# Kernel optimization log

Measured on AMD Instinct MI355X. Metric: run time of the kernel, lower is better.

## Reference

```python
import jax, jax.numpy as jnp
import numpy as np
from jax import lax

NUM_TAGS = 9
HIDDEN = 768
BATCH = 64
SEQ = 512


def setup_inputs() -> dict:
    key = jax.random.key(0)
    ks = jax.random.split(key, 6)
    hidden = jax.random.normal(ks[0], (BATCH, SEQ, HIDDEN), dtype=jnp.float32)
    labels = jax.random.randint(ks[1], (BATCH, SEQ), 0, NUM_TAGS)  # all >= 0 -> full mask
    weight = jax.random.normal(ks[2], (NUM_TAGS, HIDDEN), dtype=jnp.float32) * 0.02
    bias = jnp.zeros((NUM_TAGS,), dtype=jnp.float32)
    start_transitions = jax.random.normal(ks[3], (NUM_TAGS,), dtype=jnp.float32) * 0.1
    end_transitions = jax.random.normal(ks[4], (NUM_TAGS,), dtype=jnp.float32) * 0.1
    transitions = jax.random.normal(ks[5], (NUM_TAGS, NUM_TAGS), dtype=jnp.float32) * 0.1
    return dict(hidden=hidden, labels=labels, weight=weight, bias=bias,
                start_transitions=start_transitions, end_transitions=end_transitions,
                transitions=transitions)


def _crf_log_likelihood(emissions, tags, mask, start_t, end_t, trans):
    """pytorch-crf log-likelihood, reduction='sum'.
    emissions [B,L,T] float, tags [B,L] int, mask [B,L] bool."""
    # --- numerator: score of the gold path ---
    tag0 = tags[:, 0]
    score0 = start_t[tag0] + jnp.take_along_axis(emissions[:, 0], tag0[:, None], axis=1)[:, 0]

    def num_step(carry, inp):
        score, prev = carry
        em, tg, m = inp  # em [B,T], tg [B], m [B]
        s = trans[prev, tg] + jnp.take_along_axis(em, tg[:, None], axis=1)[:, 0]
        score = score + jnp.where(m, s, jnp.zeros_like(s))
        prev = jnp.where(m, tg, prev)
        return (score, prev), None

    (num_score, last_tag), _ = lax.scan(
        num_step, (score0, tag0),
        (emissions[:, 1:].swapaxes(0, 1), tags[:, 1:].T, mask[:, 1:].T))
    numerator = num_score + end_t[last_tag]

    # --- denominator: forward algorithm (log-sum-exp recurrence) ---
    alpha0 = start_t[None, :] + emissions[:, 0]  # [B,T]

    def den_step(alpha, inp):
        em, m = inp  # em [B,T], m [B]
        nxt = jax.nn.logsumexp(alpha[:, :, None] + trans[None], axis=1) + em
        alpha = jnp.where(m[:, None], nxt, alpha)
        return alpha, None

    alpha, _ = lax.scan(den_step, alpha0,
                        (emissions[:, 1:].swapaxes(0, 1), mask[:, 1:].T))
    denominator = jax.nn.logsumexp(alpha + end_t[None, :], axis=1)

    return jnp.sum(numerator - denominator)


def _viterbi_decode(emissions, mask, start_t, end_t, trans):
    """Max-plus DP + backtrack. Returns padded [B,L] int32 best tag sequence."""
    B, L, T = emissions.shape
    score0 = start_t[None, :] + emissions[:, 0]  # [B,T]
    identity = jnp.arange(T, dtype=jnp.int32)[None, :]  # identity backpointer for masked steps

    def fwd_step(score, inp):
        em, m = inp  # em [B,T], m [B]
        br = score[:, :, None] + trans[None]  # [B,T_prev,T_cur]
        idx = jnp.argmax(br, axis=1).astype(jnp.int32)  # [B,T]
        nxt = jnp.max(br, axis=1) + em
        score = jnp.where(m[:, None], nxt, score)
        idx = jnp.where(m[:, None], idx, identity)
        return score, idx

    final, hist = lax.scan(fwd_step, score0,
                           (emissions[:, 1:].swapaxes(0, 1), mask[:, 1:].T))
    last_tag = jnp.argmax(final + end_t[None, :], axis=1).astype(jnp.int32)  # [B]

    def back_step(tag, idx):  # idx [B,T] backpointers for this position
        prev = jnp.take_along_axis(idx, tag[:, None], axis=1)[:, 0]
        return prev, tag

    first_tag, tags_rev = lax.scan(back_step, last_tag, hist, reverse=True)
    tags = jnp.concatenate([first_tag[None, :], tags_rev], axis=0).T  # [B,L]
    return tags * mask.astype(jnp.int32)


def reference(hidden, labels, weight, bias, start_transitions, end_transitions, transitions):
    mask_full = labels >= 0
    h = hidden[:, 1:-1, :]                       # drop [CLS]/[SEP] positions
    tags = labels[:, 1:-1] * mask_full[:, 1:-1]  # zero out padded labels
    mask = mask_full[:, 1:-1]
    # dropout is identity in eval mode
    emissions = jnp.einsum('blh,th->blt', h, weight) + bias  # [B,L,T]
    llh = _crf_log_likelihood(emissions, tags, mask,
                              start_transitions, end_transitions, transitions)
    tag_seqs = _viterbi_decode(emissions, mask,
                               start_transitions, end_transitions, transitions)
    return -llh, tag_seqs.astype(jnp.float32)
```

## Files before the change

### kernel.cpp

```cpp
#include <hip/hip_runtime.h>
#include <stdint.h>

#define NB 64
#define SEQL 512
#define L 510
#define T 9
#define H 768
#define EMS 12
#define WST 388
#define LN2 0.6931471805599453f

__device__ __forceinline__ float rl(float v, int l) {
  return __uint_as_float(__builtin_amdgcn_readlane(__float_as_uint(v), l));
}

__global__ __launch_bounds__(256) void emis_kernel(
    const float* __restrict__ hidden, const float* __restrict__ weight,
    const float* __restrict__ bias, float* __restrict__ em,
    float* __restrict__ out) {
  __shared__ float4 wl[1728];
  const float4* w4 = (const float4*)weight;
  for (int k = threadIdx.x; k < 1728; k += 256) wl[k] = w4[k];
  if (blockIdx.x == 0 && threadIdx.x == 0) out[0] = 0.f;
  __syncthreads();
  const int lane = threadIdx.x & 63;
  const int wv = threadIdx.x >> 6;
  const int base = blockIdx.x * 32 + wv * 8;
  const float bj = bias[lane < 9 ? lane : 0];

  float4 ha[3], hb[3];
  {
    const int r0 = base, r1 = base + 1;
    const int b0 = r0 / L, p0 = r0 - b0 * L;
    const int b1 = r1 / L, p1 = r1 - b1 * L;
    const float4* h0 = (const float4*)(hidden + ((size_t)(b0 * SEQL + p0 + 1)) * H);
    const float4* h1 = (const float4*)(hidden + ((size_t)(b1 * SEQL + p1 + 1)) * H);
#pragma unroll
    for (int k = 0; k < 3; ++k) { ha[k] = h0[lane + 64 * k]; hb[k] = h1[lane + 64 * k]; }
  }
#pragma unroll 1
  for (int pr = 0; pr < 4; ++pr) {
    const int r0 = base + pr * 2, r1 = r0 + 1;
    float4 na[3], nb[3];
    if (pr < 3) {
      const int q0 = r0 + 2, q1 = r0 + 3;
      const int c0 = q0 / L, s0 = q0 - c0 * L;
      const int c1 = q1 / L, s1 = q1 - c1 * L;
      const float4* h0 = (const float4*)(hidden + ((size_t)(c0 * SEQL + s0 + 1)) * H);
      const float4* h1 = (const float4*)(hidden + ((size_t)(c1 * SEQL + s1 + 1)) * H);
#pragma unroll
      for (int k = 0; k < 3; ++k) { na[k] = h0[lane + 64 * k]; nb[k] = h1[lane + 64 * k]; }
    }
    float a0[T], a1[T];
#pragma unroll
    for (int t = 0; t < T; ++t) { a0[t] = 0.f; a1[t] = 0.f; }
#pragma unroll
    for (int t = 0; t < T; ++t) {
#pragma unroll
      for (int k = 0; k < 3; ++k) {
        float4 w = wl[t * 192 + lane + 64 * k];
        a0[t] = fmaf(ha[k].x, w.x, fmaf(ha[k].y, w.y, fmaf(ha[k].z, w.z, fmaf(ha[k].w, w.w, a0[t]))));
        a1[t] = fmaf(hb[k].x, w.x, fmaf(hb[k].y, w.y, fmaf(hb[k].z, w.z, fmaf(hb[k].w, w.w, a1[t]))));
      }
    }
#pragma unroll
    for (int off = 32; off; off >>= 1) {
#pragma unroll
      for (int t = 0; t < T; ++t) {
        a0[t] += __shfl_xor(a0[t], off);
        a1[t] += __shfl_xor(a1[t], off);
      }
    }
    float v0 = a0[0], v1 = a1[0];
#pragma unroll
    for (int t = 1; t < T; ++t) {
      v0 = (lane == t) ? a0[t] : v0;
      v1 = (lane == t) ? a1[t] : v1;
    }
    if (lane < 9) {
      em[(size_t)r0 * EMS + lane] = v0 + bj;
      em[(size_t)r1 * EMS + lane] = v1 + bj;
    }
#pragma unroll
    for (int k = 0; k < 3; ++k) { ha[k] = na[k]; hb[k] = nb[k]; }
  }
}

__global__ __launch_bounds__(256) void kb_kernel(
    const float* __restrict__ em, const int* __restrict__ labels,
    const float* __restrict__ start_t, const float* __restrict__ end_t,
    const float* __restrict__ trans, float* __restrict__ out) {
  __shared__ float s_emb[16 * WST];
  __shared__ float s_pd[1296];
  __shared__ float s_mv[1296];
  __shared__ float s_A[153];
  __shared__ float s_t[81];
  __shared__ float s_np[4];
  __shared__ int s_lab[L];
  __shared__ unsigned char s_ch[32];
  __shared__ uint32_t s_bp[32 * 16 * 2];
  const int b = blockIdx.x;
  const int tid = threadIdx.x;

  for (int k = tid; k < 81; k += 256) s_t[k] = trans[k];
  for (int k = tid; k < L; k += 256) s_lab[k] = labels[b * SEQL + 1 + k];
  for (int idx = tid; idx < 16 * 32 * 3; idx += 256) {
    const int s = idx / 96, rem = idx - 96 * s;
    const int r = rem / 3, c = rem - 3 * r;
    const int row = 32 * s + 1 + r;
    if (row < L) {
      float4 v = *(const float4*)(em + ((size_t)(b * L + row)) * EMS + c * 4);
      *(float4*)(s_emb + s * WST + r * 12 + c * 4) = v;
    }
  }
  __syncthreads();

  float part = 0.f;
  for (int l = tid; l < L; l += 256) {
    int tg = s_lab[l];
    float e = em[((size_t)(b * L + l)) * EMS + tg];
    if (l == 0) part += start_t[tg] + e;
    else part += s_t[s_lab[l - 1] * 9 + tg] + e;
    if (l == L - 1) part += end_t[tg];
  }
#pragma unroll
  for (int off = 32; off; off >>= 1) part += __shfl_xor(part, off);
  if ((tid & 63) == 0) s_np[tid >> 6] = part;

  const int lane = tid & 63, wv = tid >> 6;
  const int g = lane / 9;
  const int i9 = lane - g * 9;
  const bool act = g < 4;
  const int sw = wv * 4 + (act ? g : 0);
  const int ntw = (sw == 15) ? 29 : 32;
  const float* ew = s_emb + sw * WST;

  {
    float E[81];
#pragma unroll
    for (int k = 0; k < 81; ++k) E[k] = __expf(trans[k]);
    float R[9];
#pragma unroll
    for (int j = 0; j < 9; ++j) R[j] = E[i9 * 9 + j] * __expf(ew[j]);
    int iexp = 0;
    for (int t = 1; t < ntw; ++t) {
      float e[9];
#pragma unroll
      for (int j = 0; j < 9; ++j) e[j] = __expf(ew[t * 12 + j]);
      float Rn[9];
#pragma unroll
      for (int j = 0; j < 9; ++j) {
        float a = R[0] * E[0 * 9 + j];
#pragma unroll
        for (int k = 1; k < 9; ++k) a = fmaf(R[k], E[k * 9 + j], a);
        Rn[j] = a;
      }
#pragma unroll
      for (int j = 0; j < 9; ++j) R[j] = Rn[j] * e[j];
      if ((t & 3) == 0) {
        float mx = R[0];
#pragma unroll
        for (int j = 1; j < 9; ++j) mx = fmaxf(mx, R[j]);
        int ex = (int)((__float_as_uint(mx) >> 23) & 0xff) - 127;
        iexp += ex;
        float sc = __uint_as_float((uint32_t)(127 - ex) << 23);
#pragma unroll
        for (int j = 0; j < 9; ++j) R[j] *= sc;
      }
    }
    if (act) {
      float ls = (float)iexp * LN2;
#pragma unroll
      for (int j = 0; j < 9; ++j)
        s_pd[sw * 81 + j * 9 + i9] = __logf(R[j]) + ls;
    }
  }
  {
    float V[9];
#pragma unroll
    for (int j = 0; j < 9; ++j) V[j] = trans[i9 * 9 + j] + ew[j];
    for (int t = 1; t < ntw; ++t) {
      float Vn[9];
#pragma unroll
      for (int j = 0; j < 9; ++j) {
        float m = V[0] + trans[0 * 9 + j];
#pragma unroll
        for (int k = 1; k < 9; ++k) m = fmaxf(m, V[k] + trans[k * 9 + j]);
        Vn[j] = m + ew[t * 12 + j];
      }
#pragma unroll
      for (int j = 0; j < 9; ++j) V[j] = Vn[j];
    }
    if (act) {
#pragma unroll
      for (int j = 0; j < 9; ++j) s_mv[sw * 81 + j * 9 + i9] = V[j];
    }
  }
  __syncthreads();

  if (tid < 64) {
    const int jj = lane < 9 ? lane : 8;
    float D = start_t[jj] + em[(size_t)b * L * EMS + jj];
    for (int s = 0; s < 16; ++s) {
      const float* col = &s_pd[s * 81 + jj * 9];
      float v0 = rl(D, 0) + col[0], v1 = rl(D, 1) + col[1], v2 = rl(D, 2) + col[2];
      float v3 = rl(D, 3) + col[3], v4 = rl(D, 4) + col[4], v5 = rl(D, 5) + col[5];
      float v6 = rl(D, 6) + col[6], v7 = rl(D, 7) + col[7], v8 = rl(D, 8) + col[8];
      float mx = fmaxf(fmaxf(fmaxf(fmaxf(v0, v1), fmaxf(v2, v3)),
                             fmaxf(fmaxf(v4, v5), fmaxf(v6, v7))), v8);
      float sum = __expf(v0 - mx) + __expf(v1 - mx) + __expf(v2 - mx) +
                  __expf(v3 - mx) + __expf(v4 - mx) + __expf(v5 - mx) +
                  __expf(v6 - mx) + __expf(v7 - mx) + __expf(v8 - mx);
      D = mx + __logf(sum);
    }
    float fe = D + end_t[jj];
    float w0 = rl(fe, 0), w1 = rl(fe, 1), w2 = rl(fe, 2), w3 = rl(fe, 3);
    float w4 = rl(fe, 4), w5 = rl(fe, 5), w6 = rl(fe, 6), w7 = rl(fe, 7), w8 = rl(fe, 8);
    float mx = fmaxf(fmaxf(fmaxf(fmaxf(w0, w1), fmaxf(w2, w3)),
                           fmaxf(fmaxf(w4, w5), fmaxf(w6, w7))), w8);
    float den = mx + __logf(__expf(w0 - mx) + __expf(w1 - mx) + __expf(w2 - mx) +
                            __expf(w3 - mx) + __expf(w4 - mx) + __expf(w5 - mx) +
                            __expf(w6 - mx) + __expf(w7 - mx) + __expf(w8 - mx));
    if (lane == 0)
      atomicAdd(out, den - (s_np[0] + s_np[1] + s_np[2] + s_np[3]));

    float A = start_t[jj] + em[(size_t)b * L * EMS + jj];
    if (lane < 9) s_A[lane] = A;
    for (int s = 0; s < 16; ++s) {
      const float* col = &s_mv[s * 81 + jj * 9];
      float u0 = rl(A, 0) + col[0], u1 = rl(A, 1) + col[1], u2 = rl(A, 2) + col[2];
      float u3 = rl(A, 3) + col[3], u4 = rl(A, 4) + col[4], u5 = rl(A, 5) + col[5];
      float u6 = rl(A, 6) + col[6], u7 = rl(A, 7) + col[7], u8 = rl(A, 8) + col[8];
      A = fmaxf(fmaxf(fmaxf(fmaxf(u0, u1), fmaxf(u2, u3)),
                      fmaxf(fmaxf(u4, u5), fmaxf(u6, u7))), u8);
      if (lane < 9) s_A[(s + 1) * 9 + lane] = A;
    }
    float fv = A + end_t[jj];
    int j = 0;
    {
      float bv = rl(fv, 0);
#pragma unroll
      for (int i = 1; i < 9; ++i) { float v = rl(fv, i); if (v > bv) { bv = v; j = i; } }
    }
    for (int s = 15; s >= 0; --s) {
      float val = s_A[s * 9 + jj] + s_mv[s * 81 + j * 9 + jj];
      int ii = 0;
      float bb = rl(val, 0);
#pragma unroll
      for (int i = 1; i < 9; ++i) { float v = rl(val, i); if (v > bb) { bb = v; ii = i; } }
      if (lane == 0) {
        s_ch[s * 2] = (unsigned char)ii;
        s_ch[s * 2 + 1] = (unsigned char)j;
      }
      j = ii;
    }
    if (lane == 0) out[1 + (size_t)b * L] = (float)j;
  }
  __syncthreads();

  if (tid < 16) {
    const int s = tid;
    const int nt = (s == 15) ? 29 : 32;
    const int l0 = 32 * s + 1;
    const int i0 = s_ch[s * 2];
    const int jF = s_ch[s * 2 + 1];
    const float* ep = s_emb + s * WST;
    float a[9];
#pragma unroll
    for (int jx = 0; jx < 9; ++jx) a[jx] = trans[i0 * 9 + jx] + ep[jx];
    for (int q = 1; q < nt; ++q) {
      uint32_t pk0 = 0, pk1 = 0;
      float an[9];
#pragma unroll
      for (int jx = 0; jx < 9; ++jx) {
        float best = a[0] + trans[0 * 9 + jx];
        int bi = 0;
#pragma unroll
        for (int k = 1; k < 9; ++k) {
          float v = a[k] + trans[k * 9 + jx];
          if (v > best) { best = v; bi = k; }
        }
        an[jx] = best + ep[q * 12 + jx];
        if (jx < 8) pk0 |= ((uint32_t)bi) << (4 * jx);
        else pk1 = (uint32_t)bi;
      }
      s_bp[(q * 16 + s) * 2] = pk0;
      s_bp[(q * 16 + s) * 2 + 1] = pk1;
#pragma unroll
      for (int jx = 0; jx < 9; ++jx) a[jx] = an[jx];
    }
    int cur = jF;
    float* orow = out + 1 + (size_t)b * L + l0;
    for (int q = nt - 1; q >= 1; --q) {
      orow[q] = (float)cur;
      uint32_t pk = s_bp[(q * 16 + s) * 2 + (cur >> 3)];
      cur = (int)((pk >> ((cur & 7) * 4)) & 15u);
    }
    orow[0] = (float)cur;
  }
}

extern "C" void kernel_launch(void* const* d_in, const int* in_sizes, int n_in,
                              void* d_out, int out_size, void* d_ws, size_t ws_size,
                              hipStream_t stream) {
  const float* hidden  = (const float*)d_in[0];
  const int*   labels  = (const int*)d_in[1];
  const float* weight  = (const float*)d_in[2];
  const float* bias    = (const float*)d_in[3];
  const float* start_t = (const float*)d_in[4];
  const float* end_t   = (const float*)d_in[5];
  const float* trans   = (const float*)d_in[6];
  float* out = (float*)d_out;

  float* em = (float*)d_ws;

  emis_kernel<<<1020, 256, 0, stream>>>(hidden, weight, bias, em, out);
  kb_kernel<<<NB, 256, 0, stream>>>(em, labels, start_t, end_t, trans, out);
}
```

Baseline: 233.6 us.

## Run CRF sum-product and max-product chunk scans on separate waves in parallel

The kb kernel now runs 512 threads per block. The first four waves compute the log-space forward chunk matrices and the other four compute the Viterbi max-plus chunk matrices at the same time, where before one set of waves did both one after the other. Both chunk recurrences now start from an identity matrix, and the Viterbi waves cache the transition matrix in registers. The gold-path score now reads emissions from shared memory instead of global memory. The cost is a larger block and register pressure from the 81-entry arrays, and the unchanged later code in the hidden section still has to match the new wave count.

```diff
diff --git a/kernel.cpp b/kernel.cpp
--- a/kernel.cpp
+++ b/kernel.cpp
@@ -86,7 +86,7 @@
   }
 }
 
-__global__ __launch_bounds__(256) void kb_kernel(
+__global__ __launch_bounds__(512, 2) void kb_kernel(
     const float* __restrict__ em, const int* __restrict__ labels,
     const float* __restrict__ start_t, const float* __restrict__ end_t,
     const float* __restrict__ trans, float* __restrict__ out) {
@@ -95,16 +95,16 @@
   __shared__ float s_mv[1296];
   __shared__ float s_A[153];
   __shared__ float s_t[81];
-  __shared__ float s_np[4];
+  __shared__ float s_np[8];
   __shared__ int s_lab[L];
   __shared__ unsigned char s_ch[32];
   __shared__ uint32_t s_bp[32 * 16 * 2];
   const int b = blockIdx.x;
   const int tid = threadIdx.x;
 
-  for (int k = tid; k < 81; k += 256) s_t[k] = trans[k];
-  for (int k = tid; k < L; k += 256) s_lab[k] = labels[b * SEQL + 1 + k];
-  for (int idx = tid; idx < 16 * 32 * 3; idx += 256) {
+  for (int k = tid; k < 81; k += 512) s_t[k] = trans[k];
+  for (int k = tid; k < L; k += 512) s_lab[k] = labels[b * SEQL + 1 + k];
+  for (int idx = tid; idx < 16 * 32 * 3; idx += 512) {
     const int s = idx / 96, rem = idx - 96 * s;
     const int r = rem / 3, c = rem - 3 * r;
     const int row = 32 * s + 1 + r;
@@ -116,9 +116,14 @@
   __syncthreads();
 
   float part = 0.f;
-  for (int l = tid; l < L; l += 256) {
+  for (int l = tid; l < L; l += 512) {
     int tg = s_lab[l];
-    float e = em[((size_t)(b * L + l)) * EMS + tg];
+    float e;
+    if (l == 0) e = em[(size_t)b * L * EMS + tg];
+    else {
+      int s = (l - 1) >> 5, r = (l - 1) & 31;
+      e = s_emb[s * WST + r * 12 + tg];
+    }
     if (l == 0) part += start_t[tg] + e;
     else part += s_t[s_lab[l - 1] * 9 + tg] + e;
     if (l == L - 1) part += end_t[tg];
@@ -127,37 +132,38 @@
   for (int off = 32; off; off >>= 1) part += __shfl_xor(part, off);
   if ((tid & 63) == 0) s_np[tid >> 6] = part;
 
-  const int lane = tid & 63, wv = tid >> 6;
+  const int lane = tid & 63;
+  const int wvq = tid >> 6;
   const int g = lane / 9;
   const int i9 = lane - g * 9;
   const bool act = g < 4;
-  const int sw = wv * 4 + (act ? g : 0);
+  const int sw = (wvq & 3) * 4 + (act ? g : 0);
   const int ntw = (sw == 15) ? 29 : 32;
   const float* ew = s_emb + sw * WST;
 
-  {
+  if (wvq < 4) {
     float E[81];
 #pragma unroll
     for (int k = 0; k < 81; ++k) E[k] = __expf(trans[k]);
     float R[9];
 #pragma unroll
-    for (int j = 0; j < 9; ++j) R[j] = E[i9 * 9 + j] * __expf(ew[j]);
+    for (int j = 0; j < 9; ++j) R[j] = (i9 == j) ? 1.f : 0.f;
     int iexp = 0;
-    for (int t = 1; t < ntw; ++t) {
+    for (int u = 0; u < ntw; ++u) {
       float e[9];
 #pragma unroll
-      for (int j = 0; j < 9; ++j) e[j] = __expf(ew[t * 12 + j]);
+      for (int j = 0; j < 9; ++j) e[j] = __expf(ew[u * 12 + j]);
       float Rn[9];
 #pragma unroll
       for (int j = 0; j < 9; ++j) {
-        float a = R[0] * E[0 * 9 + j];
+        float a = R[0] * E[j];
 #pragma unroll
         for (int k = 1; k < 9; ++k) a = fmaf(R[k], E[k * 9 + j], a);
-        Rn[j] = a;
-      }
-#pragma unroll
-      for (int j = 0; j < 9; ++j) R[j] = Rn[j] * e[j];
-      if ((t & 3) == 0) {
+        Rn[j] = a * e[j];
+      }
+#pragma unroll
+      for (int j = 0; j < 9; ++j) R[j] = Rn[j];
+      if (u && (u & 3) == 0) {
         float mx = R[0];
 #pragma unroll
         for (int j = 1; j < 9; ++j) mx = fmaxf(mx, R[j]);
@@ -174,19 +180,21 @@
       for (int j = 0; j < 9; ++j)
         s_pd[sw * 81 + j * 9 + i9] = __logf(R[j]) + ls;
     }
-  }
-  {
+  } else {
+    float tr[81];
+#pragma unroll
+    for (int k = 0; k < 81; ++k) tr[k] = trans[k];
     float V[9];
 #pragma unroll
-    for (int j = 0; j < 9; ++j) V[j] = trans[i9 * 9 + j] + ew[j];
-    for (int t = 1; t < ntw; ++t) {
+    for (int j = 0; j < 9; ++j) V[j] = (i9 == j) ? 0.f : -1e30f;
+    for (int u = 0; u < ntw; ++u) {
       float Vn[9];
 #pragma unroll
       for (int j = 0; j < 9; ++j) {
-        float m = V[0] + trans[0 * 9 + j];
-#pragma unroll
-        for (int k = 1; k < 9; ++k) m = fmaxf(m, V[k] + trans[k * 9 + j]);
-        Vn[j] = m + ew[t * 12 + j];
+        float m = V[0] + tr[j];
+#pragma unroll
+        for (int k = 1; k < 9; ++k) m = fmaxf(m, V[k] + tr[k * 9 + j]);
+        Vn[j] = m + ew[u * 12 + j];
       }
 #pragma unroll
       for (int j = 0; j < 9; ++j) V[j] = Vn[j];
@@ -222,7 +230,8 @@
                             __expf(w3 - mx) + __expf(w4 - mx) + __expf(w5 - mx) +
                             __expf(w6 - mx) + __expf(w7 - mx) + __expf(w8 - mx));
     if (lane == 0)
-      atomicAdd(out, den - (s_np[0] + s_np[1] + s_np[2] + s_np[3]));
+      atomicAdd(out, den - (s_np[0] + s_np[1] + s_np[2] + s_np[3] +
+                            s_np[4] + s_np[5] + s_np[6] + s_np[7]));
 
     float A = start_t[jj] + em[(size_t)b * L * EMS + jj];
     if (lane < 9) s_A[lane] = A;
@@ -315,5 +324,5 @@
   float* em = (float*)d_ws;
 
   emis_kernel<<<1020, 256, 0, stream>>>(hidden, weight, bias, em, out);
-  kb_kernel<<<NB, 256, 0, stream>>>(em, labels, start_t, end_t, trans, out);
+  kb_kernel<<<NB, 512, 0, stream>>>(em, labels, start_t, end_t, trans, out);
 }
```

Result: no change. 229.2 us (-1.9%).
